# Optimization experiments

Measured on AMD Instinct MI355X. Metric: run time of the kernel, lower is better.

The kernel has to match this reference:

```python
import jax, jax.numpy as jnp
import numpy as np

DIM = 256
HEADS = 8
HEAD_DIM = DIM // HEADS
SR = 2
SCALE = HEAD_DIM ** -0.5
EPS = 1e-5
DN = ('NCHW', 'OIHW', 'NCHW')


def setup_inputs() -> dict:
    key = jax.random.key(0)
    ks = jax.random.split(key, 8)
    B, H, W = 4, 64, 64
    x = jax.random.normal(ks[0], (B, H * W, DIM), dtype=jnp.float32)
    # depthwise 3x3 convs (groups=dim): kernel [out_ch, 1, 3, 3]
    to_q_w = jax.random.normal(ks[1], (DIM, 1, 3, 3), dtype=jnp.float32) * 0.1
    to_kv_w = jax.random.normal(ks[2], (2 * DIM, 1, 3, 3), dtype=jnp.float32) * 0.1
    # spatial-reduction conv: kernel=stride=SR, with bias (torch Conv2d default)
    sr_w = jax.random.normal(ks[3], (DIM, DIM, SR, SR), dtype=jnp.float32) * 0.02
    sr_b = jax.random.normal(ks[4], (DIM,), dtype=jnp.float32) * 0.01
    ln_g = jnp.ones((DIM,), dtype=jnp.float32)
    ln_b = jnp.zeros((DIM,), dtype=jnp.float32)
    proj_w = jax.random.normal(ks[5], (DIM, DIM), dtype=jnp.float32) * 0.02
    proj_b = jax.random.normal(ks[6], (DIM,), dtype=jnp.float32) * 0.01
    return {
        'x': x, 'to_q_w': to_q_w, 'to_kv_w': to_kv_w,
        'sr_w': sr_w, 'sr_b': sr_b, 'ln_g': ln_g, 'ln_b': ln_b,
        'proj_w': proj_w, 'proj_b': proj_b, 'H': H, 'W': W,
    }


def reference(x, to_q_w, to_kv_w, sr_w, sr_b, ln_g, ln_b, proj_w, proj_b, H, W):
    B, N, C = x.shape
    x_nchw = x.reshape(B, H, W, C).transpose(0, 3, 1, 2)  # [B,C,H,W]

    # depthwise-conv Q projection (padding=1, stride=1 -> SAME)
    q = jax.lax.conv_general_dilated(x_nchw, to_q_w, (1, 1), 'SAME',
                                     feature_group_count=C, dimension_numbers=DN)
    q = q.transpose(0, 2, 3, 1).reshape(B, N, HEADS, HEAD_DIM).transpose(0, 2, 1, 3)  # [B,h,N,d]

    # spatial reduction: strided conv (kernel=stride=SR, no padding) + LayerNorm
    xr = jax.lax.conv_general_dilated(x_nchw, sr_w, (SR, SR), 'VALID',
                                      dimension_numbers=DN) + sr_b[None, :, None, None]
    Hs, Ws = xr.shape[2], xr.shape[3]
    Nk = Hs * Ws
    xr = xr.reshape(B, C, Nk).transpose(0, 2, 1)  # [B,Nk,C]
    mu = xr.mean(axis=-1, keepdims=True)
    var = ((xr - mu) ** 2).mean(axis=-1, keepdims=True)
    xr = (xr - mu) / jnp.sqrt(var + EPS) * ln_g + ln_b
    xr = xr.reshape(B, Hs, Ws, C).transpose(0, 3, 1, 2)  # [B,C,Hs,Ws]

    # depthwise-conv KV projection; torch group-major channel order out_ch=2*g+j
    kv = jax.lax.conv_general_dilated(xr, to_kv_w, (1, 1), 'SAME',
                                      feature_group_count=C, dimension_numbers=DN)
    kv = kv.transpose(0, 2, 3, 1).reshape(B, Nk, 2, HEADS, HEAD_DIM).transpose(2, 0, 3, 1, 4)
    k, v = kv[0], kv[1]  # [B,h,Nk,d]

    attn = jax.nn.softmax(jnp.einsum('bhqd,bhkd->bhqk', q, k) * SCALE, axis=-1)
    out = jnp.einsum('bhqk,bhkd->bhqd', attn, v)  # [B,h,N,d]
    out = out.transpose(0, 2, 1, 3).reshape(B, N, C)
    return out @ proj_w.T + proj_b
```

## Files before the change

kernel.cpp:

```cpp
#include <hip/hip_runtime.h>
#include <stdint.h>

typedef unsigned short u16;
typedef short s16x8 __attribute__((ext_vector_type(8)));
typedef short s16x4 __attribute__((ext_vector_type(4)));
typedef float f32x4 __attribute__((ext_vector_type(4)));
typedef uint32_t u32x4 __attribute__((ext_vector_type(4)));

#define SCALE 0.17677669529663689f
#define LOG2E 1.4426950408889634f
#define QS (SCALE * LOG2E)
#define EPS 1e-5f

static __device__ __forceinline__ u16 f2b(float f){
  uint32_t u = __float_as_uint(f);
  uint32_t r = (u + 0x7FFFu + ((u >> 16) & 1u)) >> 16;
  return (u16)r;
}
static __device__ __forceinline__ uint32_t cvtpk(float lo, float hi){
  uint32_t r;
  asm("v_cvt_pk_bf16_f32 %0, %1, %2" : "=v"(r) : "v"(lo), "v"(hi));
  return r;
}

__global__ __launch_bounds__(256) void k_prep(const float* __restrict__ srw,
                                              u16* __restrict__ wsr){
  const int t = blockIdx.x*256 + threadIdx.x;
  const int co = t >> 10, k = t & 1023;
  const float v = srw[(co<<10) + ((k&255)<<2) + (k>>8)];
  wsr[((((k>>3)<<8) + co)<<3) + (k&7)] = f2b(v);
}

__global__ __launch_bounds__(256) void k_front(const float* __restrict__ x,
                                               const float* __restrict__ qw,
                                               const float* __restrict__ pw,
                                               const u16* __restrict__ wsr,
                                               const float* __restrict__ srb,
                                               const float* __restrict__ lng,
                                               const float* __restrict__ lnb,
                                               u16* __restrict__ q,
                                               u16* __restrict__ wpj,
                                               float* __restrict__ lnxr){
  const int blk = blockIdx.x;
  const int tid = threadIdx.x;

  if (blk >= 2304){
    const int t = (blk - 2304)*256 + tid;
    const int co = t >> 8, k = t & 255;
    wpj[((((k>>3)<<8) + co)<<3) + (k&7)] = f2b(pw[(co<<8) + k]);
    return;
  }

  if (blk >= 256){
    const int qb = blk - 256;
    const int c = tid;
    const int b = qb >> 9;
    const int y = (qb >> 3) & 63;
    const int x0 = (qb & 7) << 3;
    float wv[9];
#pragma unroll
    for (int t2 = 0; t2 < 9; ++t2) wv[t2] = qw[c*9 + t2];
    float xin[3][10];
#pragma unroll
    for (int r = 0; r < 3; ++r){
      const int yy = y + r - 1;
      const bool yok = (unsigned)yy < 64u;
#pragma unroll
      for (int j = 0; j < 10; ++j){
        const int xx = x0 + j - 1;
        const bool ok = yok && ((unsigned)xx < 64u);
        xin[r][j] = ok ? x[(((b<<12) + (yy<<6) + xx) << 8) + c] : 0.f;
      }
    }
#pragma unroll
    for (int j = 0; j < 8; ++j){
      float acc = 0.f;
#pragma unroll
      for (int r = 0; r < 3; ++r)
#pragma unroll
        for (int t2 = 0; t2 < 3; ++t2)
          acc += xin[r][j+t2] * wv[r*3 + t2];
      q[(((b<<12) + (y<<6) + x0 + j) << 8) + c] = f2b(acc * QS);
    }
    return;
  }

  __shared__ float red_s[16][4], red_q[16][4];
  __shared__ float mu_s[16], rs_s[16];
  const int l = tid & 63, w = tid >> 6;
  const int r15 = l & 15, g = l >> 4;
  const int m0 = blk << 4;
  const int ma = m0 + r15;
  const int bb_ = ma >> 10, nk = ma & 1023;
  const int hs = nk >> 5, wsx = nk & 31;
  int pixbase[4];
#pragma unroll
  for (int p = 0; p < 4; ++p){
    const int y = 2*hs + (p>>1), xx = 2*wsx + (p&1);
    pixbase[p] = (((bb_<<12) + (y<<6) + xx) << 8);
  }
  f32x4 acc[4];
#pragma unroll
  for (int i = 0; i < 4; ++i) acc[i] = (f32x4){0.f,0.f,0.f,0.f};
  for (int ks = 0; ks < 32; ++ks){
    const float* ap = x + pixbase[ks>>3] + ((ks&7)<<5) + (g<<3);
    const float4 a0 = *reinterpret_cast<const float4*>(ap);
    const float4 a1 = *reinterpret_cast<const float4*>(ap + 4);
    const u32x4 apk = {cvtpk(a0.x,a0.y), cvtpk(a0.z,a0.w),
                       cvtpk(a1.x,a1.y), cvtpk(a1.z,a1.w)};
    const s16x8 af = __builtin_bit_cast(s16x8, apk);
#pragma unroll
    for (int i = 0; i < 4; ++i){
      const int co = (((w<<2)+i)<<4) + r15;
      const s16x8 bf = *reinterpret_cast<const s16x8*>(
          wsr + (((((ks<<2)+g)<<8) + co)<<3));
      acc[i] = __builtin_amdgcn_mfma_f32_16x16x32_bf16(af, bf, acc[i], 0, 0, 0);
    }
  }
  float gv[4], bv[4];
#pragma unroll
  for (int i = 0; i < 4; ++i){
    const int co = (((w<<2)+i)<<4) + r15;
    const float sb = srb[co];
    gv[i] = lng[co]; bv[i] = lnb[co];
#pragma unroll
    for (int r = 0; r < 4; ++r) acc[i][r] += sb;
  }
  float s_r[4], q_r[4];
#pragma unroll
  for (int r = 0; r < 4; ++r){
    float s = 0.f, qq = 0.f;
#pragma unroll
    for (int i = 0; i < 4; ++i){ const float v = acc[i][r]; s += v; qq += v*v; }
#pragma unroll
    for (int off = 1; off < 16; off <<= 1){
      s  += __shfl_xor(s, off);
      qq += __shfl_xor(qq, off);
    }
    s_r[r] = s; q_r[r] = qq;
  }
  if (r15 == 0){
#pragma unroll
    for (int r = 0; r < 4; ++r){
      red_s[(g<<2)+r][w] = s_r[r];
      red_q[(g<<2)+r][w] = q_r[r];
    }
  }
  __syncthreads();
  if (tid < 16){
    const float s  = red_s[tid][0]+red_s[tid][1]+red_s[tid][2]+red_s[tid][3];
    const float qq = red_q[tid][0]+red_q[tid][1]+red_q[tid][2]+red_q[tid][3];
    const float mu = s * (1.f/256.f);
    mu_s[tid] = mu;
    rs_s[tid] = rsqrtf(qq*(1.f/256.f) - mu*mu + EPS);
  }
  __syncthreads();
  float mur[4], rsr[4];
#pragma unroll
  for (int r = 0; r < 4; ++r){ mur[r] = mu_s[(g<<2)+r]; rsr[r] = rs_s[(g<<2)+r]; }
#pragma unroll
  for (int i = 0; i < 4; ++i){
    const int co = (((w<<2)+i)<<4) + r15;
#pragma unroll
    for (int r = 0; r < 4; ++r)
      lnxr[(m0+(g<<2)+r)*256 + co] = (acc[i][r]-mur[r])*rsr[r]*gv[i] + bv[i];
  }
}

__global__ __launch_bounds__(512) void k_kvconv(const float* __restrict__ lnxr,
                                                const float* __restrict__ w,
                                                u16* __restrict__ kbuf,
                                                u16* __restrict__ vT){
  const int o = threadIdx.x;
  const int blk = blockIdx.x;
  const int b = blk >> 7;
  const int y = (blk >> 2) & 31;
  const int x0 = (blk & 3) << 3;
  const int g = o >> 1;
  float wv[9];
#pragma unroll
  for (int t = 0; t < 9; ++t) wv[t] = w[o*9 + t];
  float xin[3][10];
#pragma unroll
  for (int r = 0; r < 3; ++r){
    const int yy = y + r - 1;
    const bool yok = (unsigned)yy < 32u;
#pragma unroll
    for (int j = 0; j < 10; ++j){
      const int xx = x0 + j - 1;
      const bool ok = yok && ((unsigned)xx < 32u);
      xin[r][j] = ok ? lnxr[(((b<<10) + (yy<<5) + xx) << 8) + g] : 0.f;
    }
  }
  float acc[8];
#pragma unroll
  for (int j = 0; j < 8; ++j){
    float a = 0.f;
#pragma unroll
    for (int r = 0; r < 3; ++r)
#pragma unroll
      for (int t = 0; t < 3; ++t)
        a += xin[r][j+t] * wv[r*3 + t];
    acc[j] = a;
  }
  const int t = o & 255;
  const int h = t >> 5, dd = t & 31;
  if (o < 256){
    const int nkbase = (((b<<3) + h) << 10) + (y<<5) + x0;
#pragma unroll
    for (int j = 0; j < 8; ++j)
      kbuf[((nkbase + j) << 5) + dd] = f2b(acc[j]);
  } else {
    s16x8 pack;
#pragma unroll
    for (int j = 0; j < 8; ++j) pack[j] = (short)f2b(acc[j]);
    const int col0 = (y<<5) + x0;
    const int colS = (((col0>>3) ^ (dd&7)) << 3);
    *reinterpret_cast<s16x8*>(
        vT + (((((b<<3) + h) << 5) + dd) << 10) + colS) = pack;
  }
}

__global__ __launch_bounds__(1024, 4) void k_attn(const u16* __restrict__ q,
                                                  const u16* __restrict__ kbuf,
                                                  const u16* __restrict__ vT,
                                                  u16* __restrict__ attb){
  __shared__ __align__(16) u16 KL[32768];
  __shared__ __align__(16) u16 VL[32768];
  const int tid = threadIdx.x;
  const int l = tid & 63, w = tid >> 6;
  const int i = blockIdx.x;
  const int xcd = i & 7, slot = i >> 3;
  const int bh = (xcd<<2) + (slot>>3);
  const int chunk = slot & 7;
  const int b = bh >> 3, h = bh & 7;
  const int r15 = l & 15, g = l >> 4;
  const int n0 = (chunk<<9) + (w<<5);

  {
    const uint4* kg = (const uint4*)(kbuf + (bh<<15));
    const uint4* vg = (const uint4*)(vT   + (bh<<15));
    uint4* kl = (uint4*)KL;
    uint4* vl = (uint4*)VL;
#pragma unroll
    for (int r = 0; r < 4; ++r){
      kl[(r<<10) + tid] = kg[(r<<10) + tid];
      vl[(r<<10) + tid] = vg[(r<<10) + tid];
    }
  }
  __syncthreads();

  s16x8 qf[2];
#pragma unroll
  for (int qi = 0; qi < 2; ++qi)
    qf[qi] = *reinterpret_cast<const s16x8*>(
        q + (((b<<12) + n0 + (qi<<4) + r15) << 8) + (h<<5) + (g<<3));

  f32x4 acc[2][2];
#pragma unroll
  for (int qi = 0; qi < 2; ++qi){
    acc[qi][0] = (f32x4){0.f,0.f,0.f,0.f};
    acc[qi][1] = (f32x4){0.f,0.f,0.f,0.f};
  }
  const f32x4 zero = {0.f,0.f,0.f,0.f};
  float lsum[2] = {0.f,0.f};
  const int vswz = (r15 & 7);

  for (int kv0 = 0; kv0 < 1024; kv0 += 64){
    s16x8 kf[4];
#pragma unroll
    for (int st = 0; st < 4; ++st)
      kf[st] = *reinterpret_cast<const s16x8*>(
          KL + ((kv0 + (st<<4) + r15) << 5) + (g<<3));
    s16x8 vf[2][2];
#pragma unroll
    for (int pr = 0; pr < 2; ++pr)
#pragma unroll
      for (int h2 = 0; h2 < 2; ++h2){
        const int cl  = kv0 + (pr<<5) + (g<<2);
        const int cl2 = cl + 16;
        const int rb  = ((h2<<4) + r15) << 10;
        const s16x4 v0 = *reinterpret_cast<const s16x4*>(
            VL + rb + (((cl >>3) ^ vswz) << 3) + (cl &7));
        const s16x4 v1 = *reinterpret_cast<const s16x4*>(
            VL + rb + (((cl2>>3) ^ vswz) << 3) + (cl2&7));
        s16x8 vv;
        vv[0]=v0[0]; vv[1]=v0[1]; vv[2]=v0[2]; vv[3]=v0[3];
        vv[4]=v1[0]; vv[5]=v1[1]; vv[6]=v1[2]; vv[7]=v1[3];
        vf[pr][h2] = vv;
      }
#pragma unroll
    for (int qi = 0; qi < 2; ++qi){
      f32x4 s[4];
      __builtin_amdgcn_s_setprio(1);
#pragma unroll
      for (int st = 0; st < 4; ++st)
        s[st] = __builtin_amdgcn_mfma_f32_16x16x32_bf16(kf[st], qf[qi], zero, 0, 0, 0);
      __builtin_amdgcn_s_setprio(0);
      float p[4][4];
      float ps = 0.f;
#pragma unroll
      for (int st = 0; st < 4; ++st)
#pragma unroll
        for (int r = 0; r < 4; ++r){
          const float e = __builtin_amdgcn_exp2f(s[st][r]);
          p[st][r] = e;
          ps += e;
        }
      ps += __shfl_xor(ps, 16);
      ps += __shfl_xor(ps, 32);
      lsum[qi] += ps;
      const u32x4 pk0 = {cvtpk(p[0][0],p[0][1]), cvtpk(p[0][2],p[0][3]),
                         cvtpk(p[1][0],p[1][1]), cvtpk(p[1][2],p[1][3])};
      const u32x4 pk1 = {cvtpk(p[2][0],p[2][1]), cvtpk(p[2][2],p[2][3]),
                         cvtpk(p[3][0],p[3][1]), cvtpk(p[3][2],p[3][3])};
      const s16x8 pf0 = __builtin_bit_cast(s16x8, pk0);
      const s16x8 pf1 = __builtin_bit_cast(s16x8, pk1);
      __builtin_amdgcn_s_setprio(1);
#pragma unroll
      for (int h2 = 0; h2 < 2; ++h2){
        acc[qi][h2] = __builtin_amdgcn_mfma_f32_16x16x32_bf16(pf0, vf[0][h2], acc[qi][h2], 0, 0, 0);
        acc[qi][h2] = __builtin_amdgcn_mfma_f32_16x16x32_bf16(pf1, vf[1][h2], acc[qi][h2], 0, 0, 0);
      }
      __builtin_amdgcn_s_setprio(0);
    }
  }
#pragma unroll
  for (int qi = 0; qi < 2; ++qi){
    const float linv = 1.f / lsum[qi];
#pragma unroll
    for (int r = 0; r < 4; ++r){
      const float fl = __shfl(linv, (g<<2) + r);
      const int n = n0 + (qi<<4) + (g<<2) + r;
      u16* orow = attb + (((b<<12) + n) << 8) + (h<<5) + r15;
      orow[0]  = f2b(acc[qi][0][r] * fl);
      orow[16] = f2b(acc[qi][1][r] * fl);
    }
  }
}

__global__ __launch_bounds__(256) void k_proj(const u16* __restrict__ attb,
                                              const u16* __restrict__ wpj,
                                              const float* __restrict__ pb,
                                              float* __restrict__ out){
  const int tid = threadIdx.x;
  const int l = tid & 63, w = tid >> 6;
  const int r15 = l & 15, g = l >> 4;
  const int m0 = blockIdx.x << 4;
  f32x4 acc[4];
#pragma unroll
  for (int i = 0; i < 4; ++i) acc[i] = (f32x4){0.f,0.f,0.f,0.f};
  const u16* arow = attb + (m0 + r15)*256 + (g<<3);
#pragma unroll
  for (int ks = 0; ks < 8; ++ks){
    const s16x8 af = *reinterpret_cast<const s16x8*>(arow + (ks<<5));
#pragma unroll
    for (int i = 0; i < 4; ++i){
      const int co = (((w<<2)+i)<<4) + r15;
      const s16x8 bf = *reinterpret_cast<const s16x8*>(
          wpj + (((((ks<<2)+g)<<8) + co)<<3));
      acc[i] = __builtin_amdgcn_mfma_f32_16x16x32_bf16(af, bf, acc[i], 0, 0, 0);
    }
  }
#pragma unroll
  for (int i = 0; i < 4; ++i){
    const int co = (((w<<2)+i)<<4) + r15;
    const float pbv = pb[co];
#pragma unroll
    for (int r = 0; r < 4; ++r)
      out[(m0+(g<<2)+r)*256 + co] = acc[i][r] + pbv;
  }
}

extern "C" void kernel_launch(void* const* d_in, const int* in_sizes, int n_in,
                              void* d_out, int out_size, void* d_ws, size_t ws_size,
                              hipStream_t stream){
  const float* x   = (const float*)d_in[0];
  const float* qw  = (const float*)d_in[1];
  const float* kvw = (const float*)d_in[2];
  const float* srw = (const float*)d_in[3];
  const float* srb = (const float*)d_in[4];
  const float* lng = (const float*)d_in[5];
  const float* lnb = (const float*)d_in[6];
  const float* pw  = (const float*)d_in[7];
  const float* pb  = (const float*)d_in[8];
  float* out = (float*)d_out;

  char* ws = (char*)d_ws;
  u16*   qbuf = (u16*)(ws);
  u16*   attb = (u16*)(ws + 8388608);
  float* lnxr = (float*)(ws + 16777216);
  u16*   kbuf = (u16*)(ws + 20971520);
  u16*   vT   = (u16*)(ws + 23068672);
  u16*   wsr  = (u16*)(ws + 25165824);
  u16*   wpj  = (u16*)(ws + 25690112);

  hipLaunchKernelGGL(k_prep,   dim3(1024), dim3(256),  0, stream, srw, wsr);
  hipLaunchKernelGGL(k_front,  dim3(2560), dim3(256),  0, stream,
                     x, qw, pw, wsr, srb, lng, lnb, qbuf, wpj, lnxr);
  hipLaunchKernelGGL(k_kvconv, dim3(512),  dim3(512),  0, stream, lnxr, kvw, kbuf, vT);
  hipLaunchKernelGGL(k_attn,   dim3(256),  dim3(1024), 0, stream, qbuf, kbuf, vT, attb);
  hipLaunchKernelGGL(k_proj,   dim3(1024), dim3(256),  0, stream, attb, wpj, pb, out);
}
```

Measured before the change: 77.76 us.

## Halve attention block size, give each wave 64 queries, defer row-sum shuffles

The attention kernel now runs 512-thread blocks where each wave handles 64 query rows (four 16-row tiles) instead of 32. Each K and V fragment read from LDS is reused across twice as many queries, which cuts LDS traffic per query. The per-iteration cross-lane shuffles for the softmax denominator move to a single reduction after the loop, and the kv loop is unrolled by two. The cost is more registers per thread and half as many waves per block, which lowers latency hiding.

```diff
diff --git a/kernel.cpp b/kernel.cpp
--- a/kernel.cpp
+++ b/kernel.cpp
@@ -221,10 +221,10 @@
   }
 }
 
-__global__ __launch_bounds__(1024, 4) void k_attn(const u16* __restrict__ q,
-                                                  const u16* __restrict__ kbuf,
-                                                  const u16* __restrict__ vT,
-                                                  u16* __restrict__ attb){
+__global__ __launch_bounds__(512) void k_attn(const u16* __restrict__ q,
+                                              const u16* __restrict__ kbuf,
+                                              const u16* __restrict__ vT,
+                                              u16* __restrict__ attb){
   __shared__ __align__(16) u16 KL[32768];
   __shared__ __align__(16) u16 VL[32768];
   const int tid = threadIdx.x;
@@ -235,7 +235,7 @@
   const int chunk = slot & 7;
   const int b = bh >> 3, h = bh & 7;
   const int r15 = l & 15, g = l >> 4;
-  const int n0 = (chunk<<9) + (w<<5);
+  const int n0 = (chunk<<9) + (w<<6);
 
   {
     const uint4* kg = (const uint4*)(kbuf + (bh<<15));
@@ -243,29 +243,30 @@
     uint4* kl = (uint4*)KL;
     uint4* vl = (uint4*)VL;
 #pragma unroll
-    for (int r = 0; r < 4; ++r){
-      kl[(r<<10) + tid] = kg[(r<<10) + tid];
-      vl[(r<<10) + tid] = vg[(r<<10) + tid];
+    for (int r = 0; r < 8; ++r){
+      kl[(r<<9) + tid] = kg[(r<<9) + tid];
+      vl[(r<<9) + tid] = vg[(r<<9) + tid];
     }
   }
   __syncthreads();
 
-  s16x8 qf[2];
-#pragma unroll
-  for (int qi = 0; qi < 2; ++qi)
+  s16x8 qf[4];
+#pragma unroll
+  for (int qi = 0; qi < 4; ++qi)
     qf[qi] = *reinterpret_cast<const s16x8*>(
         q + (((b<<12) + n0 + (qi<<4) + r15) << 8) + (h<<5) + (g<<3));
 
-  f32x4 acc[2][2];
-#pragma unroll
-  for (int qi = 0; qi < 2; ++qi){
+  f32x4 acc[4][2];
+#pragma unroll
+  for (int qi = 0; qi < 4; ++qi){
     acc[qi][0] = (f32x4){0.f,0.f,0.f,0.f};
     acc[qi][1] = (f32x4){0.f,0.f,0.f,0.f};
   }
   const f32x4 zero = {0.f,0.f,0.f,0.f};
-  float lsum[2] = {0.f,0.f};
+  float lsum[4] = {0.f,0.f,0.f,0.f};
   const int vswz = (r15 & 7);
 
+#pragma unroll 2
   for (int kv0 = 0; kv0 < 1024; kv0 += 64){
     s16x8 kf[4];
 #pragma unroll
@@ -290,30 +291,25 @@
         vf[pr][h2] = vv;
       }
 #pragma unroll
-    for (int qi = 0; qi < 2; ++qi){
+    for (int qi = 0; qi < 4; ++qi){
       f32x4 s[4];
       __builtin_amdgcn_s_setprio(1);
 #pragma unroll
       for (int st = 0; st < 4; ++st)
         s[st] = __builtin_amdgcn_mfma_f32_16x16x32_bf16(kf[st], qf[qi], zero, 0, 0, 0);
       __builtin_amdgcn_s_setprio(0);
-      float p[4][4];
-      float ps = 0.f;
+      f32x4 e[4];
 #pragma unroll
       for (int st = 0; st < 4; ++st)
 #pragma unroll
-        for (int r = 0; r < 4; ++r){
-          const float e = __builtin_amdgcn_exp2f(s[st][r]);
-          p[st][r] = e;
-          ps += e;
-        }
-      ps += __shfl_xor(ps, 16);
-      ps += __shfl_xor(ps, 32);
-      lsum[qi] += ps;
-      const u32x4 pk0 = {cvtpk(p[0][0],p[0][1]), cvtpk(p[0][2],p[0][3]),
-                         cvtpk(p[1][0],p[1][1]), cvtpk(p[1][2],p[1][3])};
-      const u32x4 pk1 = {cvtpk(p[2][0],p[2][1]), cvtpk(p[2][2],p[2][3]),
-                         cvtpk(p[3][0],p[3][1]), cvtpk(p[3][2],p[3][3])};
+        for (int r = 0; r < 4; ++r)
+          e[st][r] = __builtin_amdgcn_exp2f(s[st][r]);
+      const f32x4 sum4 = (e[0] + e[1]) + (e[2] + e[3]);
+      lsum[qi] += (sum4[0] + sum4[1]) + (sum4[2] + sum4[3]);
+      const u32x4 pk0 = {cvtpk(e[0][0],e[0][1]), cvtpk(e[0][2],e[0][3]),
+                         cvtpk(e[1][0],e[1][1]), cvtpk(e[1][2],e[1][3])};
+      const u32x4 pk1 = {cvtpk(e[2][0],e[2][1]), cvtpk(e[2][2],e[2][3]),
+                         cvtpk(e[3][0],e[3][1]), cvtpk(e[3][2],e[3][3])};
       const s16x8 pf0 = __builtin_bit_cast(s16x8, pk0);
       const s16x8 pf1 = __builtin_bit_cast(s16x8, pk1);
       __builtin_amdgcn_s_setprio(1);
@@ -326,7 +322,12 @@
     }
   }
 #pragma unroll
-  for (int qi = 0; qi < 2; ++qi){
+  for (int qi = 0; qi < 4; ++qi){
+    lsum[qi] += __shfl_xor(lsum[qi], 16);
+    lsum[qi] += __shfl_xor(lsum[qi], 32);
+  }
+#pragma unroll
+  for (int qi = 0; qi < 4; ++qi){
     const float linv = 1.f / lsum[qi];
 #pragma unroll
     for (int r = 0; r < 4; ++r){
@@ -395,10 +396,10 @@
   u16*   wsr  = (u16*)(ws + 25165824);
   u16*   wpj  = (u16*)(ws + 25690112);
 
-  hipLaunchKernelGGL(k_prep,   dim3(1024), dim3(256),  0, stream, srw, wsr);
-  hipLaunchKernelGGL(k_front,  dim3(2560), dim3(256),  0, stream,
+  hipLaunchKernelGGL(k_prep,   dim3(1024), dim3(256), 0, stream, srw, wsr);
+  hipLaunchKernelGGL(k_front,  dim3(2560), dim3(256), 0, stream,
                      x, qw, pw, wsr, srb, lng, lnb, qbuf, wpj, lnxr);
-  hipLaunchKernelGGL(k_kvconv, dim3(512),  dim3(512),  0, stream, lnxr, kvw, kbuf, vT);
-  hipLaunchKernelGGL(k_attn,   dim3(256),  dim3(1024), 0, stream, qbuf, kbuf, vT, attb);
-  hipLaunchKernelGGL(k_proj,   dim3(1024), dim3(256),  0, stream, attb, wpj, pb, out);
-}
+  hipLaunchKernelGGL(k_kvconv, dim3(512),  dim3(512), 0, stream, lnxr, kvw, kbuf, vT);
+  hipLaunchKernelGGL(k_attn,   dim3(256),  dim3(512), 0, stream, qbuf, kbuf, vT, attb);
+  hipLaunchKernelGGL(k_proj,   dim3(1024), dim3(256), 0, stream, attb, wpj, pb, out);
+}
```

New measurement: 77.16 us. About the same (-0.8%).
